# Optimization experiments

Measured on AMD Instinct MI355X. Metric: run time of the kernel, lower is better.

The kernel has to match this reference:

```python
import jax, jax.numpy as jnp
import numpy as np

# dims: batch, points, patches(groups), patch size, hidden, heads, layers, ffn
B, N, G, K, D, H, L, F = 32, 8192, 256, 32, 384, 6, 12, 1536
MASK_RATIO = 0.75
LEN_KEEP = int(G * (1 - MASK_RATIO))  # 64 visible tokens
HD = D // H


def _layernorm(x, g, b, eps=1e-5):
    m = jnp.mean(x, -1, keepdims=True)
    v = jnp.mean(jnp.square(x - m), -1, keepdims=True)
    return (x - m) * jax.lax.rsqrt(v + eps) * g + b


def _normalize_points(x):
    # normalize(): center = mid of bbox, radius = max distance to center (iso/diag)
    bmin = x.min(-2, keepdims=True)
    bmax = x.max(-2, keepdims=True)
    center = 0.5 * (bmin + bmax)
    radius = jnp.linalg.norm(x - center, axis=-1, keepdims=True).max(-2, keepdims=True)
    return (x - center) / radius


def _fps(x, num_samples):
    # farthest point sampling; sequential by nature -> fori_loop over G (fixed, small)
    b, n, _ = x.shape
    idxs = jnp.zeros((b, num_samples), jnp.int32)

    def body(i, state):
        dists, idxs, last = state
        lastpt = jnp.take_along_axis(x, last[:, None, None].astype(jnp.int32), axis=1)  # [B,1,3]
        d = jnp.sum(jnp.square(x - lastpt), -1)  # [B,N]
        dists = jnp.minimum(dists, d)
        nxt = jnp.argmax(dists, -1).astype(jnp.int32)
        return dists, idxs.at[:, i].set(nxt), nxt

    dists0 = jnp.full((b, n), 1e10, x.dtype)
    _, idxs, _ = jax.lax.fori_loop(1, num_samples, body, (dists0, idxs, jnp.zeros((b,), jnp.int32)))
    return idxs


def _group(x, centers):
    # squared pairwise distances without materializing [B,G,N,3]
    d2 = (jnp.sum(jnp.square(centers), -1)[:, :, None]
          + jnp.sum(jnp.square(x), -1)[:, None, :]
          - 2.0 * jnp.einsum('bgc,bnc->bgn', centers, x))  # [B,G,N]
    _, idx = jax.lax.top_k(-d2, K)  # [B,G,K] knn indices
    nbrs = jnp.take_along_axis(x[:, None, :, :], idx[..., None], axis=2)  # [B,G,K,3] (_knn_gather)
    return nbrs - centers[:, :, None, :]


def setup_inputs() -> dict:
    key = jax.random.key(0)
    ks = iter(jax.random.split(key, 24))

    def w(shape, scale=0.02):
        return jax.random.normal(next(ks), shape, jnp.float32) * scale

    ones_ln = jnp.stack([jnp.ones(D, jnp.float32), jnp.zeros(D, jnp.float32)])
    return {
        'points': jax.random.normal(next(ks), (B, N, 3), jnp.float32),
        'noise': jax.random.uniform(next(ks), (B, G), jnp.float32),
        # mini-PointNet patch encoder
        'pe_w1': w((3, 128)), 'pe_b1': jnp.zeros((128,), jnp.float32),
        'pe_w2': w((128, 256)), 'pe_b2': jnp.zeros((256,), jnp.float32),
        'pe_w3': w((256, D)), 'pe_b3': jnp.zeros((D,), jnp.float32),
        # positional MLP on patch centers
        'pos_w1': w((3, 128)), 'pos_b1': jnp.zeros((128,), jnp.float32),
        'pos_w2': w((128, D)), 'pos_b2': jnp.zeros((D,), jnp.float32),
        # transformer (stacked over L layers)
        'ln1': jnp.tile(ones_ln[None], (L, 1, 1)),
        'wqkv': w((L, D, 3 * D)), 'bqkv': jnp.zeros((L, 3 * D), jnp.float32),
        'wo': w((L, D, D)), 'bo': jnp.zeros((L, D), jnp.float32),
        'ln2': jnp.tile(ones_ln[None], (L, 1, 1)),
        'wi': w((L, D, F)), 'bi': jnp.zeros((L, F), jnp.float32),
        'wo2': w((L, F, D)), 'bo2': jnp.zeros((L, D), jnp.float32),
        'lnf': ones_ln,
    }


def _forward(points, noise, pe_w1, pe_b1, pe_w2, pe_b2, pe_w3, pe_b3,
             pos_w1, pos_b1, pos_w2, pos_b2,
             ln1, wqkv, bqkv, wo, bo, ln2, wi, bi, wo2, bo2, lnf):
    x = _normalize_points(points)
    cidx = _fps(x, G)                                        # [B,G]
    centers = jnp.take_along_axis(x, cidx[..., None], axis=1)  # [B,G,3]
    patches = _group(x, centers)                              # [B,G,K,3]

    # patch encode (per-point MLP -> max pool -> proj)
    f = jax.nn.relu(patches @ pe_w1 + pe_b1)
    f = f @ pe_w2 + pe_b2
    tokens = f.max(axis=2) @ pe_w3 + pe_b3                    # [B,G,D]
    pos = jax.nn.relu(centers @ pos_w1 + pos_b1) @ pos_w2 + pos_b2  # [B,G,D]

    # mask(): argsort-of-noise shuffle, keep first len_keep tokens
    ids_shuffle = jnp.argsort(noise, axis=1)
    ids_keep = ids_shuffle[:, :LEN_KEEP]                      # [B,64]
    h = (jnp.take_along_axis(tokens, ids_keep[..., None], axis=1)
         + jnp.take_along_axis(pos, ids_keep[..., None], axis=1))  # [B,64,D]

    scale = 1.0 / jnp.sqrt(jnp.asarray(HD, h.dtype))

    def layer(h, p):
        l1, wq, bq, wo_, bo_, l2, wi_, bi_, wo2_, bo2_ = p
        y = _layernorm(h, l1[0], l1[1])
        qkv = (y @ wq + bq).reshape(B, LEN_KEEP, 3, H, HD)  # '(three h d)' split
        q, k, v = jnp.moveaxis(qkv, 2, 0)
        a = jax.nn.softmax(jnp.einsum('bshd,bthd->bhst', q, k) * scale, -1)
        o = jnp.einsum('bhst,bthd->bshd', a, v).reshape(B, LEN_KEEP, D)
        h = h + o @ wo_ + bo_
        y = _layernorm(h, l2[0], l2[1])
        h = h + jax.nn.gelu(y @ wi_ + bi_) @ wo2_ + bo2_
        return h, None

    h, _ = jax.lax.scan(layer, h, (ln1, wqkv, bqkv, wo, bo, ln2, wi, bi, wo2, bo2))
    return _layernorm(h, lnf[0], lnf[1])


def reference(points, noise, pe_w1, pe_b1, pe_w2, pe_b2, pe_w3, pe_b3,
              pos_w1, pos_b1, pos_w2, pos_b2,
              ln1, wqkv, bqkv, wo, bo, ln2, wi, bi, wo2, bo2, lnf):
    return _forward(points, noise, pe_w1, pe_b1, pe_w2, pe_b2, pe_w3, pe_b3,
                    pos_w1, pos_b1, pos_w2, pos_b2,
                    ln1, wqkv, bqkv, wo, bo, ln2, wi, bi, wo2, bo2, lnf)
```

## Files before the change

kernel.cpp:

```cpp
#include <hip/hip_runtime.h>

#define NPTS 8192
#define NB   32
#define NG   256
#define NK   32
#define ND   384
#define NH   6
#define NLK  64
#define NF   1536
#define NHD  64
#define NL   12
#define MM   2048

typedef unsigned short u16;
typedef unsigned long long u64;
typedef __attribute__((ext_vector_type(8))) short short8;
typedef __attribute__((ext_vector_type(16))) float f32x16;
typedef __attribute__((ext_vector_type(4))) unsigned short ushort4v;

__device__ __forceinline__ float bf2f(u16 v){
  unsigned int u = ((unsigned int)v) << 16;
  float f; __builtin_memcpy(&f, &u, 4); return f;
}
__device__ __forceinline__ float ldf(const void* p, size_t i, bool bf){
  if(bf) return bf2f(((const u16*)p)[i]);
  return ((const float*)p)[i];
}
__device__ __forceinline__ u16 f2bf(float f){
  unsigned int x; __builtin_memcpy(&x, &f, 4);
  x += 0x7fffu + ((x >> 16) & 1u);
  return (u16)(x >> 16);
}
__device__ __forceinline__ void split2(float v, u16& hi, u16& lo){
  hi = f2bf(v);
  lo = f2bf(v - bf2f(hi));
}

__global__ __launch_bounds__(256) void k_detect(const u16* __restrict__ pts,
                                                int* __restrict__ flag){
  __shared__ int bad;
  if(threadIdx.x==0) bad=0;
  __syncthreads();
  int hit=0;
  for(int i=threadIdx.x; i<4096; i+=256){
    unsigned e = (pts[i] >> 7) & 0xFFu;
    if(e >= 0x90u) hit=1;
  }
  if(hit) atomicOr(&bad, 1);
  __syncthreads();
  if(threadIdx.x==0) *flag = bad ? 0 : 1;
}

__device__ __forceinline__ float blockMax256(float v, float* sb, int tid){
  for(int off=32; off; off>>=1) v = fmaxf(v, __shfl_down(v, off));
  __syncthreads();
  if((tid&63)==0) sb[tid>>6] = v;
  __syncthreads();
  return fmaxf(fmaxf(sb[0],sb[1]), fmaxf(sb[2],sb[3]));
}

__global__ __launch_bounds__(256) void k_normalize(const void* __restrict__ pts,
                                                   float* __restrict__ xn,
                                                   const int* __restrict__ flag){
#pragma clang fp contract(off)
  int b = blockIdx.x, tid = threadIdx.x;
  const bool bf = flag[0] != 0;
  __shared__ float sb[4];
  const size_t base = (size_t)b*NPTS*3;
  float mn0=1e30f,mn1=1e30f,mn2=1e30f, mx0=-1e30f,mx1=-1e30f,mx2=-1e30f;
  for(int n=tid; n<NPTS; n+=256){
    float x0=ldf(pts,base+n*3,bf), x1=ldf(pts,base+n*3+1,bf), x2=ldf(pts,base+n*3+2,bf);
    mn0=fminf(mn0,x0); mx0=fmaxf(mx0,x0);
    mn1=fminf(mn1,x1); mx1=fmaxf(mx1,x1);
    mn2=fminf(mn2,x2); mx2=fmaxf(mx2,x2);
  }
  mx0=blockMax256(mx0,sb,tid); mn0=-blockMax256(-mn0,sb,tid);
  mx1=blockMax256(mx1,sb,tid); mn1=-blockMax256(-mn1,sb,tid);
  mx2=blockMax256(mx2,sb,tid); mn2=-blockMax256(-mn2,sb,tid);
  float c0=0.5f*(mn0+mx0), c1=0.5f*(mn1+mx1), c2=0.5f*(mn2+mx2);
  float mr=0.0f;
  for(int n=tid; n<NPTS; n+=256){
    float d0=ldf(pts,base+n*3,bf)-c0, d1=ldf(pts,base+n*3+1,bf)-c1, d2=ldf(pts,base+n*3+2,bf)-c2;
    float nr = sqrtf((d0*d0 + d1*d1) + d2*d2);
    mr = fmaxf(mr, nr);
  }
  float radius = blockMax256(mr, sb, tid);
  float* XO = xn + base;
  for(int n=tid; n<NPTS; n+=256){
    XO[n*3  ] = (ldf(pts,base+n*3  ,bf)-c0)/radius;
    XO[n*3+1] = (ldf(pts,base+n*3+1,bf)-c1)/radius;
    XO[n*3+2] = (ldf(pts,base+n*3+2,bf)-c2)/radius;
  }
}

__global__ __launch_bounds__(256) void k_keep(const void* __restrict__ noise,
                                              int* __restrict__ keep,
                                              const int* __restrict__ flag){
  int b = blockIdx.x, g = threadIdx.x;
  const bool bf = flag[0] != 0;
  __shared__ float nv[NG];
  nv[g] = ldf(noise, (size_t)b*NG+g, bf);
  __syncthreads();
  float v = nv[g]; int r = 0;
  for(int j=0; j<NG; j++){
    float u = nv[j];
    r += (u < v) || (u == v && j < g);
  }
  if(r < NLK) keep[b*NLK + r] = g;
}

__device__ __forceinline__ void kmax_dpp_step(unsigned& hi, unsigned& lo, unsigned oh, unsigned ol){
  bool g = (oh > hi) || (oh == hi && ol > lo);
  hi = g ? oh : hi; lo = g ? ol : lo;
}
#define KMAX_DPP(CTRL) { \
  unsigned oh=(unsigned)__builtin_amdgcn_update_dpp(0,(int)kh,(CTRL),0xf,0xf,true); \
  unsigned ol=(unsigned)__builtin_amdgcn_update_dpp(0,(int)kl,(CTRL),0xf,0xf,true); \
  kmax_dpp_step(kh,kl,oh,ol); }

__global__ __launch_bounds__(512) void k_fps(const float* __restrict__ xn,
                                             float* __restrict__ centers){
#pragma clang fp contract(off)
  int b = blockIdx.x, tid = threadIdx.x;
  int lane = tid & 63;
  const float* X = xn + (size_t)b*NPTS*3;
  __shared__ float xs[NPTS*3];
  __shared__ u64 skey[3];
  __shared__ int sc[NG];
  float px[16],py[16],pz[16],dd[16];
#pragma unroll
  for(int s=0;s<16;s++){
    int n = s*512 + tid;
    px[s]=X[n*3]; py[s]=X[n*3+1]; pz[s]=X[n*3+2];
    dd[s]=1e10f;
  }
  for(int i=tid; i<NPTS*3; i+=512) xs[i] = X[i];
  if(tid==0){ skey[0]=0ull; skey[1]=0ull; skey[2]=0ull; sc[0]=0; }
  __syncthreads();
  float lx = xs[0], ly = xs[1], lz = xs[2];
  for(int i=1;i<NG;i++){
    int c = i % 3;
    float bv=-1.0f; int bs=0;
#pragma unroll
    for(int s=0;s<16;s++){
      float dx=px[s]-lx, dy=py[s]-ly, dz=pz[s]-lz;
      float d=(dx*dx + dy*dy) + dz*dz;
      d = fminf(dd[s], d); dd[s]=d;
      if(d > bv){ bv=d; bs=s; }
    }
    int bn = bs*512 + tid;
    unsigned kh; __builtin_memcpy(&kh,&bv,4);
    unsigned kl = (unsigned)(NPTS-1-bn);
    KMAX_DPP(0x111)
    KMAX_DPP(0x112)
    KMAX_DPP(0x114)
    KMAX_DPP(0x118)
    KMAX_DPP(0x142)
    KMAX_DPP(0x143)
    if(lane==63) atomicMax(&skey[c], ((u64)kh<<32) | (u64)kl);
    __syncthreads();
    u64 k64 = skey[c];
    int n = (NPTS-1) - (int)(k64 & 0xFFFFFFFFull);
    n &= (NPTS-1);
    if(tid==0){ sc[i]=n; skey[(i+2)%3]=0ull; }
    lx = xs[n*3]; ly = xs[n*3+1]; lz = xs[n*3+2];
  }
  __syncthreads();
  if(tid < NG){
    int n = sc[tid] & (NPTS-1);
    centers[((size_t)b*NG+tid)*3  ] = xs[n*3];
    centers[((size_t)b*NG+tid)*3+1] = xs[n*3+1];
    centers[((size_t)b*NG+tid)*3+2] = xs[n*3+2];
  }
}

__global__ __launch_bounds__(256) void k_knn(
    const float* __restrict__ xn, const float* __restrict__ centers,
    const int* __restrict__ keep, float* __restrict__ patches)
{
  int blk=blockIdx.x; int b=blk>>6; int j=blk&63; int tid=threadIdx.x;
  __shared__ float sd[NPTS];
  __shared__ int   sel[NK];
  __shared__ float rv[4]; __shared__ int rn[4];
  __shared__ int   sseln;
  int g = keep[b*NLK + j] & (NG-1);
  const float* C = centers + ((size_t)b*NG + g)*3;
  float c0=C[0], c1=C[1], c2=C[2];
  const float* X = xn + (size_t)b*NPTS*3;
  {
#pragma clang fp contract(off)
    float cc = (c0*c0 + c1*c1) + c2*c2;
    for(int n=tid; n<NPTS; n+=256){
      float x0=X[n*3], x1=X[n*3+1], x2=X[n*3+2];
      float xx=(x0*x0 + x1*x1) + x2*x2;
      float dt=(c0*x0 + c1*x1) + c2*x2;
      sd[n] = (cc + xx) - 2.0f*dt;
    }
  }
  __syncthreads();
  float dl[32];
  for(int s=0;s<32;s++) dl[s] = sd[s*256 + tid];
  unsigned int alive = 0xffffffffu;
  for(int r=0; r<NK; r++){
    float bv=1e30f; int bn=0x7fffffff;
    for(int s=0;s<32;s++){
      if(alive & (1u<<s)){
        float v = dl[s];
        if(v < bv){ bv=v; bn=s*256+tid; }
      }
    }
    for(int off=32;off;off>>=1){
      float ov=__shfl_down(bv,off); int on=__shfl_down(bn,off);
      if(ov<bv || (ov==bv && on<bn)){ bv=ov; bn=on; }
    }
    if((tid&63)==0){ rv[tid>>6]=bv; rn[tid>>6]=bn; }
    __syncthreads();
    if(tid==0){
      float v=rv[0]; int n=rn[0];
      for(int w=1;w<4;w++) if(rv[w]<v || (rv[w]==v && rn[w]<n)){ v=rv[w]; n=rn[w]; }
      n &= (NPTS-1);
      sseln=n; sel[r]=n;
    }
    __syncthreads();
    int n = sseln;
    if((n & 255) == tid) alive &= ~(1u << (n >> 8));
  }
  __syncthreads();
  if(tid < NK){
    int n = sel[tid] & (NPTS-1);
    float* P = patches + ((size_t)(b*NLK+j)*NK + tid)*3;
    P[0]=X[n*3  ]-c0;
    P[1]=X[n*3+1]-c1;
    P[2]=X[n*3+2]-c2;
  }
}

__global__ __launch_bounds__(256) void k_embed(
    const float* __restrict__ patches, const float* __restrict__ centers,
    const int* __restrict__ keep,
    const void* __restrict__ w1, const void* __restrict__ b1,
    const void* __restrict__ w2, const void* __restrict__ b2,
    const void* __restrict__ pw1, const void* __restrict__ pb1,
    u16* __restrict__ mfhi, u16* __restrict__ mflo,
    u16* __restrict__ phhi, u16* __restrict__ phlo,
    const int* __restrict__ flag)
{
  int blk=blockIdx.x; int b=blk>>6; int j=blk&63; int tid=threadIdx.x;
  const bool bf = flag[0] != 0;
  __shared__ float pat[NK*3];
  __shared__ __align__(16) float f1t[128*36];
  int row = b*NLK + j;
  if(tid < NK*3) pat[tid] = patches[(size_t)row*NK*3 + tid];
  __syncthreads();
  for(int i=0;i<16;i++){
    int idx = tid + i*256;
    int k = idx>>7, m = idx&127;
    float v = ldf(b1,m,bf)
            + pat[k*3+0]*ldf(w1,        m,bf)
            + pat[k*3+1]*ldf(w1, 128 + m,bf)
            + pat[k*3+2]*ldf(w1, 256 + m,bf);
    f1t[m*36 + k] = fmaxf(v, 0.0f);
  }
  __syncthreads();
  float acc[NK];
  {
    float bv = ldf(b2, tid, bf);
#pragma unroll
    for(int k=0;k<NK;k++) acc[k]=bv;
  }
  for(int jj=0;jj<128;jj++){
    float wv = ldf(w2, (size_t)jj*256+tid, bf);
    const float* fr = &f1t[jj*36];
#pragma unroll
    for(int k8=0;k8<8;k8++){
      float4 fv = *reinterpret_cast<const float4*>(fr + k8*4);
      acc[k8*4+0] = fmaf(fv.x, wv, acc[k8*4+0]);
      acc[k8*4+1] = fmaf(fv.y, wv, acc[k8*4+1]);
      acc[k8*4+2] = fmaf(fv.z, wv, acc[k8*4+2]);
      acc[k8*4+3] = fmaf(fv.w, wv, acc[k8*4+3]);
    }
  }
  float mx = acc[0];
#pragma unroll
  for(int k=1;k<NK;k++) mx = fmaxf(mx, acc[k]);
  { u16 hi,lo; split2(mx,hi,lo);
    mfhi[(size_t)row*256 + tid]=hi; mflo[(size_t)row*256 + tid]=lo; }
  if(tid < 128){
    int g = keep[b*NLK + j] & (NG-1);
    const float* C = centers + ((size_t)b*NG + g)*3;
    float v = ldf(pb1,tid,bf)
            + C[0]*ldf(pw1,        tid,bf)
            + C[1]*ldf(pw1, 128 + tid,bf)
            + C[2]*ldf(pw1, 256 + tid,bf);
    v = fmaxf(v, 0.0f);
    u16 hi,lo; split2(v,hi,lo);
    phhi[(size_t)row*128 + tid]=hi; phlo[(size_t)row*128 + tid]=lo;
  }
}

__global__ __launch_bounds__(256) void k_transpose(const void* __restrict__ W, size_t woff,
    int Kd, int Nd, u16* __restrict__ dhi, u16* __restrict__ dlo, size_t doff,
    const int* __restrict__ flag){
  __shared__ float t[32][33];
  const bool bf = flag[0]!=0;
  int n0 = blockIdx.x*32, k0 = blockIdx.y*32;
  for(int i=0;i<4;i++){
    int idx = threadIdx.x + i*256; int kr = idx>>5, nc = idx&31;
    t[kr][nc] = ldf(W, woff + (size_t)(k0+kr)*Nd + n0+nc, bf);
  }
  __syncthreads();
  for(int i=0;i<4;i++){
    int idx = threadIdx.x + i*256; int nr = idx>>5, kc = idx&31;
    float v = t[kc][nr];
    u16 hi,lo; split2(v,hi,lo);
    size_t o = doff + (size_t)(n0+nr)*Kd + k0+kc;
    dhi[o]=hi; dlo[o]=lo;
  }
}

__global__ __launch_bounds__(256) void k_transpose4(
    const void* __restrict__ wqkv, const void* __restrict__ wo,
    const void* __restrict__ wi,   const void* __restrict__ wo2,
    int l, u16* __restrict__ dhi, u16* __restrict__ dlo,
    const int* __restrict__ flag){
  __shared__ float t[32][33];
  const bool bf = flag[0]!=0;
  int id = blockIdx.x;
  const void* W; int Kd, Nd; size_t woff, doff; int local;
  if(id < 432){        W=wqkv; Kd=384;  Nd=1152; woff=(size_t)l*442368; doff=0;       local=id; }
  else if(id < 576){   W=wo;   Kd=384;  Nd=384;  woff=(size_t)l*147456; doff=442368;  local=id-432; }
  else if(id < 1152){  W=wi;   Kd=384;  Nd=1536; woff=(size_t)l*589824; doff=589824;  local=id-576; }
  else {               W=wo2;  Kd=1536; Nd=384;  woff=(size_t)l*589824; doff=1179648; local=id-1152; }
  int ntiles = Nd >> 5;
  int n0 = (local % ntiles)*32, k0 = (local / ntiles)*32;
  for(int i=0;i<4;i++){
    int idx = threadIdx.x + i*256; int kr = idx>>5, nc = idx&31;
    t[kr][nc] = ldf(W, woff + (size_t)(k0+kr)*Nd + n0+nc, bf);
  }
  __syncthreads();
  for(int i=0;i<4;i++){
    int idx = threadIdx.x + i*256; int nr = idx>>5, kc = idx&31;
    float v = t[kc][nr];
    u16 hi,lo; split2(v,hi,lo);
    size_t o = doff + (size_t)(n0+nr)*Kd + k0+kc;
    dhi[o]=hi; dlo[o]=lo;
  }
}

__global__ __launch_bounds__(128) void k_ln_split(const float* __restrict__ X,
                                                  const void* __restrict__ gb, size_t go,
                                                  u16* __restrict__ Yhi, u16* __restrict__ Ylo,
                                                  const int* __restrict__ flag){
  int row=blockIdx.x, tid=threadIdx.x;
  const bool bf = flag[0] != 0;
  const float* x = X + (size_t)row*ND;
  __shared__ float sbuf[2];
  float v0=x[tid], v1=x[tid+128], v2=x[tid+256];
  float s = v0+v1+v2;
  for(int off=32;off;off>>=1) s += __shfl_down(s,off);
  if((tid&63)==0) sbuf[tid>>6]=s;
  __syncthreads();
  float mean = (sbuf[0]+sbuf[1]) * (1.0f/(float)ND);
  __syncthreads();
  float d0=v0-mean, d1=v1-mean, d2=v2-mean;
  s = d0*d0 + d1*d1 + d2*d2;
  for(int off=32;off;off>>=1) s += __shfl_down(s,off);
  if((tid&63)==0) sbuf[tid>>6]=s;
  __syncthreads();
  float var = (sbuf[0]+sbuf[1]) * (1.0f/(float)ND);
  float rstd = 1.0f / sqrtf(var + 1e-5f);
  float o0 = d0*rstd*ldf(gb,go+tid    ,bf) + ldf(gb,go+ND+tid    ,bf);
  float o1 = d1*rstd*ldf(gb,go+tid+128,bf) + ldf(gb,go+ND+tid+128,bf);
  float o2 = d2*rstd*ldf(gb,go+tid+256,bf) + ldf(gb,go+ND+tid+256,bf);
  u16 hi,lo; size_t rb = (size_t)row*ND;
  split2(o0,hi,lo); Yhi[rb+tid    ]=hi; Ylo[rb+tid    ]=lo;
  split2(o1,hi,lo); Yhi[rb+tid+128]=hi; Ylo[rb+tid+128]=lo;
  split2(o2,hi,lo); Yhi[rb+tid+256]=hi; Ylo[rb+tid+256]=lo;
}

template<int TM, int TN, int ACT, bool RES, bool OSPLIT>
__global__ __launch_bounds__(256) void k_gemm_mfma(
    const u16* __restrict__ Ahi, const u16* __restrict__ Alo,
    const u16* __restrict__ Whi, const u16* __restrict__ Wlo, size_t wo,
    const void* __restrict__ bias, size_t bo, const int* __restrict__ flag,
    const float* __restrict__ res, float* __restrict__ Cf,
    u16* __restrict__ Ohi, u16* __restrict__ Olo,
    int N, int K)
{
  __shared__ __align__(16) u16 sAh[2][64*40];
  __shared__ __align__(16) u16 sAl[2][64*40];
  __shared__ __align__(16) u16 sBh[2][64*40];
  __shared__ __align__(16) u16 sBl[2][64*40];
  int tid = threadIdx.x;
  int wave = tid >> 6, lane = tid & 63;
  int wm = wave >> 1, wn = wave & 1;
  int l31 = lane & 31, half = lane >> 5;
  int row0 = blockIdx.y*TM, col0 = blockIdx.x*TN;
  const bool bf = flag[0] != 0;
  f32x16 acc;
#pragma unroll
  for(int r=0;r<16;r++) acc[r]=0.f;

  const int sr  = tid >> 2;
  const int scc = (tid & 3) * 8;
  const u16* gAh = Ahi + (size_t)(row0+sr)*K + scc;
  const u16* gAl = Alo + (size_t)(row0+sr)*K + scc;
  const u16* gBh = Whi + wo + (size_t)(col0+sr)*K + scc;
  const u16* gBl = Wlo + wo + (size_t)(col0+sr)*K + scc;
  const int ldst = sr*40 + scc;

  uint4 rah = *reinterpret_cast<const uint4*>(gAh);
  uint4 ral = *reinterpret_cast<const uint4*>(gAl);
  uint4 rbh = *reinterpret_cast<const uint4*>(gBh);
  uint4 rbl = *reinterpret_cast<const uint4*>(gBl);

  const int nk = K >> 5;
  for(int t=0; t<nk; ++t){
    const int buf = t & 1;
    *reinterpret_cast<uint4*>(&sAh[buf][ldst]) = rah;
    *reinterpret_cast<uint4*>(&sAl[buf][ldst]) = ral;
    *reinterpret_cast<uint4*>(&sBh[buf][ldst]) = rbh;
    *reinterpret_cast<uint4*>(&sBl[buf][ldst]) = rbl;
    __syncthreads();
    if(t+1 < nk){
      const int ko = (t+1) << 5;
      rah = *reinterpret_cast<const uint4*>(gAh + ko);
      ral = *reinterpret_cast<const uint4*>(gAl + ko);
      rbh = *reinterpret_cast<const uint4*>(gBh + ko);
      rbl = *reinterpret_cast<const uint4*>(gBl + ko);
    }
#pragma unroll
    for(int ks=0; ks<2; ks++){
      int aoff = (wm*32 + l31)*40 + ks*16 + half*8;
      int boff = (wn*32 + l31)*40 + ks*16 + half*8;
      short8 ah = *reinterpret_cast<const short8*>(&sAh[buf][aoff]);
      short8 al = *reinterpret_cast<const short8*>(&sAl[buf][aoff]);
      short8 bh = *reinterpret_cast<const short8*>(&sBh[buf][boff]);
      short8 bl = *reinterpret_cast<const short8*>(&sBl[buf][boff]);
      acc = __builtin_amdgcn_mfma_f32_32x32x16_bf16(ah, bh, acc, 0,0,0);
      acc = __builtin_amdgcn_mfma_f32_32x32x16_bf16(ah, bl, acc, 0,0,0);
      acc = __builtin_amdgcn_mfma_f32_32x32x16_bf16(al, bh, acc, 0,0,0);
    }
  }
  int col = col0 + wn*32 + l31;
  float bv = ldf(bias, bo+col, bf);
#pragma unroll
  for(int r=0;r<16;r++){
    int row = row0 + wm*32 + (r&3) + 8*(r>>2) + 4*half;
    float v = acc[r] + bv;
    if(ACT==1){
      float xx = v;
      v = 0.5f*xx*(1.0f + tanhf(0.7978845608028654f*(xx + 0.044715f*xx*xx*xx)));
    }
    if(RES) v += res[(size_t)row*N + col];
    if(OSPLIT){
      u16 hi,lo; split2(v,hi,lo);
      Ohi[(size_t)row*N + col]=hi; Olo[(size_t)row*N + col]=lo;
    }else{
      Cf[(size_t)row*N + col]=v;
    }
  }
}

__global__ __launch_bounds__(256) void k_attn_pl(const float* __restrict__ qkv,
                                                 u16* __restrict__ ohi,
                                                 u16* __restrict__ olo){
  __shared__ float Qt[64*68];
  __shared__ float Kt[64*68];
  __shared__ float V [64*68];
  __shared__ float SB[64*68];
  int blk=blockIdx.x; int b=blk/NH, h=blk%NH;
  int tid=threadIdx.x;
  for(int idx=tid; idx<4096; idx+=256){
    int s=idx>>6, d=idx&63;
    const float* r = qkv + ((size_t)(b*NLK+s))*1152 + h*NHD + d;
    Qt[d*68+s]=r[0];
    Kt[d*68+s]=r[384];
    V [s*68+d]=r[768];
  }
  __syncthreads();
  {
    const int i0 = (tid>>4)*4, j0 = (tid&15)*4;
    float a00=0.f,a01=0.f,a02=0.f,a03=0.f;
    float a10=0.f,a11=0.f,a12=0.f,a13=0.f;
    float a20=0.f,a21=0.f,a22=0.f,a23=0.f;
    float a30=0.f,a31=0.f,a32=0.f,a33=0.f;
#pragma unroll 4
    for(int d=0;d<64;d++){
      float4 qa = *reinterpret_cast<const float4*>(&Qt[d*68+i0]);
      float4 kb = *reinterpret_cast<const float4*>(&Kt[d*68+j0]);
      a00=fmaf(qa.x,kb.x,a00); a01=fmaf(qa.x,kb.y,a01); a02=fmaf(qa.x,kb.z,a02); a03=fmaf(qa.x,kb.w,a03);
      a10=fmaf(qa.y,kb.x,a10); a11=fmaf(qa.y,kb.y,a11); a12=fmaf(qa.y,kb.z,a12); a13=fmaf(qa.y,kb.w,a13);
      a20=fmaf(qa.z,kb.x,a20); a21=fmaf(qa.z,kb.y,a21); a22=fmaf(qa.z,kb.z,a22); a23=fmaf(qa.z,kb.w,a23);
      a30=fmaf(qa.w,kb.x,a30); a31=fmaf(qa.w,kb.y,a31); a32=fmaf(qa.w,kb.z,a32); a33=fmaf(qa.w,kb.w,a33);
    }
    float4 o0 = {a00*0.125f, a01*0.125f, a02*0.125f, a03*0.125f};
    float4 o1 = {a10*0.125f, a11*0.125f, a12*0.125f, a13*0.125f};
    float4 o2 = {a20*0.125f, a21*0.125f, a22*0.125f, a23*0.125f};
    float4 o3 = {a30*0.125f, a31*0.125f, a32*0.125f, a33*0.125f};
    *reinterpret_cast<float4*>(&SB[(i0  )*68+j0]) = o0;
    *reinterpret_cast<float4*>(&SB[(i0+1)*68+j0]) = o1;
    *reinterpret_cast<float4*>(&SB[(i0+2)*68+j0]) = o2;
    *reinterpret_cast<float4*>(&SB[(i0+3)*68+j0]) = o3;
  }
  __syncthreads();
  if(tid<64){
    float* rowp=&SB[tid*68];
    float m=rowp[0];
    for(int j=1;j<64;j++) m=fmaxf(m,rowp[j]);
    float sum=0.0f;
    for(int j=0;j<64;j++){ float e=__expf(rowp[j]-m); rowp[j]=e; sum+=e; }
    for(int j=0;j<64;j++) Qt[j*68+tid] = rowp[j]/sum;
  }
  __syncthreads();
  {
    const int s0 = (tid>>4)*4, d0 = (tid&15)*4;
    float a00=0.f,a01=0.f,a02=0.f,a03=0.f;
    float a10=0.f,a11=0.f,a12=0.f,a13=0.f;
    float a20=0.f,a21=0.f,a22=0.f,a23=0.f;
    float a30=0.f,a31=0.f,a32=0.f,a33=0.f;
#pragma unroll 4
    for(int t=0;t<64;t++){
      float4 av = *reinterpret_cast<const float4*>(&Qt[t*68+s0]);
      float4 vv = *reinterpret_cast<const float4*>(&V [t*68+d0]);
      a00=fmaf(av.x,vv.x,a00); a01=fmaf(av.x,vv.y,a01); a02=fmaf(av.x,vv.z,a02); a03=fmaf(av.x,vv.w,a03);
      a10=fmaf(av.y,vv.x,a10); a11=fmaf(av.y,vv.y,a11); a12=fmaf(av.y,vv.z,a12); a13=fmaf(av.y,vv.w,a13);
      a20=fmaf(av.z,vv.x,a20); a21=fmaf(av.z,vv.y,a21); a22=fmaf(av.z,vv.z,a22); a23=fmaf(av.z,vv.w,a23);
      a30=fmaf(av.w,vv.x,a30); a31=fmaf(av.w,vv.y,a31); a32=fmaf(av.w,vv.z,a32); a33=fmaf(av.w,vv.w,a33);
    }
    float rr[4][4] = {{a00,a01,a02,a03},{a10,a11,a12,a13},{a20,a21,a22,a23},{a30,a31,a32,a33}};
#pragma unroll
    for(int si=0; si<4; si++){
      ushort4v h4, l4;
#pragma unroll
      for(int di=0; di<4; di++){
        u16 hi,lo; split2(rr[si][di],hi,lo);
        h4[di]=hi; l4[di]=lo;
      }
      size_t o = ((size_t)(b*NLK+s0+si))*ND + h*NHD + d0;
      *reinterpret_cast<ushort4v*>(&ohi[o]) = h4;
      *reinterpret_cast<ushort4v*>(&olo[o]) = l4;
    }
  }
}

template<bool FINAL>
__global__ __launch_bounds__(128) void k_ln(const float* __restrict__ X,
                                            const void* __restrict__ gb, size_t go,
                                            void* __restrict__ Y,
                                            const int* __restrict__ flag){
  int row=blockIdx.x, tid=threadIdx.x;
  const bool bf = flag[0] != 0;
  const float* x = X + (size_t)row*ND;
  __shared__ float sbuf[2];
  float v0=x[tid], v1=x[tid+128], v2=x[tid+256];
  float s = v0+v1+v2;
  for(int off=32;off;off>>=1) s += __shfl_down(s,off);
  if((tid&63)==0) sbuf[tid>>6]=s;
  __syncthreads();
  float mean = (sbuf[0]+sbuf[1]) * (1.0f/(float)ND);
  __syncthreads();
  float d0=v0-mean, d1=v1-mean, d2=v2-mean;
  s = d0*d0 + d1*d1 + d2*d2;
  for(int off=32;off;off>>=1) s += __shfl_down(s,off);
  if((tid&63)==0) sbuf[tid>>6]=s;
  __syncthreads();
  float var = (sbuf[0]+sbuf[1]) * (1.0f/(float)ND);
  float rstd = 1.0f / sqrtf(var + 1e-5f);
  float o0 = d0*rstd*ldf(gb,go+tid    ,bf) + ldf(gb,go+ND+tid    ,bf);
  float o1 = d1*rstd*ldf(gb,go+tid+128,bf) + ldf(gb,go+ND+tid+128,bf);
  float o2 = d2*rstd*ldf(gb,go+tid+256,bf) + ldf(gb,go+ND+tid+256,bf);
  if(FINAL && bf){
    u16* yo = (u16*)Y + (size_t)row*ND;
    yo[tid]=f2bf(o0); yo[tid+128]=f2bf(o1); yo[tid+256]=f2bf(o2);
  }else{
    float* yo = (float*)Y + (size_t)row*ND;
    yo[tid]=o0; yo[tid+128]=o1; yo[tid+256]=o2;
  }
}

extern "C" void kernel_launch(void* const* d_in, const int* in_sizes, int n_in,
                              void* d_out, int out_size, void* d_ws, size_t ws_size,
                              hipStream_t stream){
  (void)in_sizes; (void)n_in; (void)out_size;
  const void* pts   = d_in[0];
  const void* noise = d_in[1];
  const void* pe_w1 = d_in[2];
  const void* pe_b1 = d_in[3];
  const void* pe_w2 = d_in[4];
  const void* pe_b2 = d_in[5];
  const void* pe_w3 = d_in[6];
  const void* pe_b3 = d_in[7];
  const void* pos_w1= d_in[8];
  const void* pos_b1= d_in[9];
  const void* pos_w2= d_in[10];
  const void* pos_b2= d_in[11];
  const void* ln1   = d_in[12];
  const void* wqkv  = d_in[13];
  const void* bqkv  = d_in[14];
  const void* wo    = d_in[15];
  const void* bo    = d_in[16];
  const void* ln2   = d_in[17];
  const void* wi    = d_in[18];
  const void* bi    = d_in[19];
  const void* wo2   = d_in[20];
  const void* bo2   = d_in[21];
  const void* lnf   = d_in[22];

  const size_t needed_new = (6711296ull + 16) * 4;
  if (ws_size < needed_new) return;

  float* ws   = (float*)d_ws;
  float* h    = ws;
  u16*  yhi   = (u16*)(ws + 786432);
  u16*  ylo   = yhi + 786432;
  float* qkvb = ws + 1572864;
  u16*  athi  = (u16*)(ws + 3932160);
  u16*  atlo  = athi + 786432;
  u16*  ubhi  = (u16*)(ws + 1572864);
  u16*  ublo  = ubhi + 3145728;
  float* xn   = ws + 1572864;
  u16*  wthi  = (u16*)(ws + 4718592);
  u16*  wtlo  = wthi + 1769472;
  float* patches = ws + 6488064;
  float* centers = ws + 6684672;
  int*   keep    = (int*)(ws + 6709248);
  u16*  mfhi  = yhi;            u16* mflo = yhi + 2048*256;
  u16*  phhi  = athi;           u16* phlo = athi + 2048*128;
  int*   flag = (int*)(ws + 6711296);

  k_detect   <<<1, 256, 0, stream>>>((const u16*)pts, flag);
  k_normalize<<<NB, 256, 0, stream>>>(pts, xn, flag);
  k_keep     <<<NB, 256, 0, stream>>>(noise, keep, flag);
  k_fps      <<<NB, 512, 0, stream>>>(xn, centers);
  k_knn      <<<NB*NLK, 256, 0, stream>>>(xn, centers, keep, patches);
  k_embed    <<<NB*NLK, 256, 0, stream>>>(patches, centers, keep,
      pe_w1, pe_b1, pe_w2, pe_b2, pos_w1, pos_b1,
      mfhi, mflo, phhi, phlo, flag);
  k_transpose<<<dim3(12, 8), 256, 0, stream>>>(pe_w3, 0, 256, 384, wthi, wtlo, 0, flag);
  k_transpose<<<dim3(12, 4), 256, 0, stream>>>(pos_w2, 0, 128, 384, wthi, wtlo, 98304, flag);
  k_gemm_mfma<64,64,0,false,false><<<dim3(6,32), 256, 0, stream>>>(
      mfhi, mflo, wthi, wtlo, 0, pe_b3, 0, flag, nullptr, h, nullptr, nullptr, 384, 256);
  k_gemm_mfma<64,64,0,true ,false><<<dim3(6,32), 256, 0, stream>>>(
      phhi, phlo, wthi, wtlo, 98304, pos_b2, 0, flag, h, h, nullptr, nullptr, 384, 128);

  for(int l=0; l<NL; l++){
    k_transpose4<<<1728, 256, 0, stream>>>(wqkv, wo, wi, wo2, l, wthi, wtlo, flag);

    k_ln_split<<<MM, 128, 0, stream>>>(h, ln1, (size_t)l*2*ND, yhi, ylo, flag);
    k_gemm_mfma<64,64,0,false,false><<<dim3(18,32), 256, 0, stream>>>(
        yhi, ylo, wthi, wtlo, 0, bqkv, (size_t)l*1152, flag, nullptr, qkvb, nullptr, nullptr, 1152, 384);
    k_attn_pl<<<NB*NH, 256, 0, stream>>>(qkvb, athi, atlo);
    k_gemm_mfma<64,64,0,true ,false><<<dim3(6,32), 256, 0, stream>>>(
        athi, atlo, wthi, wtlo, 442368, bo, (size_t)l*384, flag, h, h, nullptr, nullptr, 384, 384);
    k_ln_split<<<MM, 128, 0, stream>>>(h, ln2, (size_t)l*2*ND, yhi, ylo, flag);
    k_gemm_mfma<64,64,1,false,true ><<<dim3(24,32), 256, 0, stream>>>(
        yhi, ylo, wthi, wtlo, 589824, bi, (size_t)l*1536, flag, nullptr, nullptr, ubhi, ublo, 1536, 384);
    k_gemm_mfma<64,64,0,true ,false><<<dim3(6,32), 256, 0, stream>>>(
        ubhi, ublo, wthi, wtlo, 1179648, bo2, (size_t)l*384, flag, h, h, nullptr, nullptr, 384, 1536);
  }
  k_ln<true><<<MM, 128, 0, stream>>>(h, lnf, 0, d_out, flag);
}
```

Baseline: 1.872 ms.

## Overlap all weight transposes with FPS in one fused launch

Extends the FPS kernel with extra blocks that transpose and hi/lo-split all embedding and all 12 layers' weights into a persistent buffer while the 32 FPS blocks run. This removes the per-layer transpose launches from the serial layer chain and uses CUs left idle by the latency-bound FPS. It requires a larger workspace. It falls back to per-layer transposes when the workspace is too small, and the fallback rearranges buffer offsets.

```diff
diff --git a/kernel.cpp b/kernel.cpp
--- a/kernel.cpp
+++ b/kernel.cpp
@@ -17,6 +17,10 @@
 typedef __attribute__((ext_vector_type(8))) short short8;
 typedef __attribute__((ext_vector_type(16))) float f32x16;
 typedef __attribute__((ext_vector_type(4))) unsigned short ushort4v;
+
+#define PL_PRE   147456ull
+#define PL_LAYER 1769472ull
+#define WT_ELEMS (PL_PRE + 12ull*PL_LAYER)
 
 __device__ __forceinline__ float bf2f(u16 v){
   unsigned int u = ((unsigned int)v) << 16;
@@ -118,59 +122,101 @@
   unsigned ol=(unsigned)__builtin_amdgcn_update_dpp(0,(int)kl,(CTRL),0xf,0xf,true); \
   kmax_dpp_step(kh,kl,oh,ol); }
 
-__global__ __launch_bounds__(512) void k_fps(const float* __restrict__ xn,
-                                             float* __restrict__ centers){
-#pragma clang fp contract(off)
-  int b = blockIdx.x, tid = threadIdx.x;
-  int lane = tid & 63;
-  const float* X = xn + (size_t)b*NPTS*3;
+__global__ __launch_bounds__(512) void k_fps_trans(
+    const float* __restrict__ xn, float* __restrict__ centers,
+    const void* __restrict__ pe_w3, const void* __restrict__ pos_w2,
+    const void* __restrict__ wqkv, const void* __restrict__ wo,
+    const void* __restrict__ wi,   const void* __restrict__ wo2,
+    u16* __restrict__ wthi, u16* __restrict__ wtlo,
+    const int* __restrict__ flag)
+{
   __shared__ float xs[NPTS*3];
   __shared__ u64 skey[3];
   __shared__ int sc[NG];
-  float px[16],py[16],pz[16],dd[16];
-#pragma unroll
-  for(int s=0;s<16;s++){
-    int n = s*512 + tid;
-    px[s]=X[n*3]; py[s]=X[n*3+1]; pz[s]=X[n*3+2];
-    dd[s]=1e10f;
-  }
-  for(int i=tid; i<NPTS*3; i+=512) xs[i] = X[i];
-  if(tid==0){ skey[0]=0ull; skey[1]=0ull; skey[2]=0ull; sc[0]=0; }
-  __syncthreads();
-  float lx = xs[0], ly = xs[1], lz = xs[2];
-  for(int i=1;i<NG;i++){
-    int c = i % 3;
-    float bv=-1.0f; int bs=0;
+  int tid = threadIdx.x;
+
+  if(blockIdx.x >= 32){
+    const bool bf = flag[0]!=0;
+    float (*t)[33] = reinterpret_cast<float(*)[33]>(xs);
+    int gid = blockIdx.x - 32;
+    const void* W; int Kd, Nd; size_t woff, doff; int local;
+    if(gid < 96){        W=pe_w3;  Kd=256; Nd=384; woff=0; doff=0;      local=gid; }
+    else if(gid < 144){  W=pos_w2; Kd=128; Nd=384; woff=0; doff=98304;  local=gid-96; }
+    else{
+      int g2 = gid - 144; int l = g2 / 1728; int id = g2 % 1728;
+      size_t lb = PL_PRE + (size_t)l*PL_LAYER;
+      if(id < 432){        W=wqkv; Kd=384;  Nd=1152; woff=(size_t)l*442368; doff=lb;          local=id; }
+      else if(id < 576){   W=wo;   Kd=384;  Nd=384;  woff=(size_t)l*147456; doff=lb+442368;   local=id-432; }
+      else if(id < 1152){  W=wi;   Kd=384;  Nd=1536; woff=(size_t)l*589824; doff=lb+589824;   local=id-576; }
+      else {               W=wo2;  Kd=1536; Nd=384;  woff=(size_t)l*589824; doff=lb+1179648;  local=id-1152; }
+    }
+    int ntiles = Nd >> 5;
+    int n0 = (local % ntiles)*32, k0 = (local / ntiles)*32;
+    for(int i=0;i<2;i++){
+      int idx = tid + i*512; int kr = idx>>5, nc = idx&31;
+      t[kr][nc] = ldf(W, woff + (size_t)(k0+kr)*Nd + n0+nc, bf);
+    }
+    __syncthreads();
+    for(int i=0;i<2;i++){
+      int idx = tid + i*512; int nr = idx>>5, kc = idx&31;
+      float v = t[kc][nr];
+      u16 hi,lo; split2(v,hi,lo);
+      size_t o = doff + (size_t)(n0+nr)*Kd + k0+kc;
+      wthi[o]=hi; wtlo[o]=lo;
+    }
+    return;
+  }
+
+  {
+#pragma clang fp contract(off)
+    int b = blockIdx.x;
+    int lane = tid & 63;
+    const float* X = xn + (size_t)b*NPTS*3;
+    float px[16],py[16],pz[16],dd[16];
 #pragma unroll
     for(int s=0;s<16;s++){
-      float dx=px[s]-lx, dy=py[s]-ly, dz=pz[s]-lz;
-      float d=(dx*dx + dy*dy) + dz*dz;
-      d = fminf(dd[s], d); dd[s]=d;
-      if(d > bv){ bv=d; bs=s; }
-    }
-    int bn = bs*512 + tid;
-    unsigned kh; __builtin_memcpy(&kh,&bv,4);
-    unsigned kl = (unsigned)(NPTS-1-bn);
-    KMAX_DPP(0x111)
-    KMAX_DPP(0x112)
-    KMAX_DPP(0x114)
-    KMAX_DPP(0x118)
-    KMAX_DPP(0x142)
-    KMAX_DPP(0x143)
-    if(lane==63) atomicMax(&skey[c], ((u64)kh<<32) | (u64)kl);
+      int n = s*512 + tid;
+      px[s]=X[n*3]; py[s]=X[n*3+1]; pz[s]=X[n*3+2];
+      dd[s]=1e10f;
+    }
+    for(int i=tid; i<NPTS*3; i+=512) xs[i] = X[i];
+    if(tid==0){ skey[0]=0ull; skey[1]=0ull; skey[2]=0ull; sc[0]=0; }
     __syncthreads();
-    u64 k64 = skey[c];
-    int n = (NPTS-1) - (int)(k64 & 0xFFFFFFFFull);
-    n &= (NPTS-1);
-    if(tid==0){ sc[i]=n; skey[(i+2)%3]=0ull; }
-    lx = xs[n*3]; ly = xs[n*3+1]; lz = xs[n*3+2];
-  }
-  __syncthreads();
-  if(tid < NG){
-    int n = sc[tid] & (NPTS-1);
-    centers[((size_t)b*NG+tid)*3  ] = xs[n*3];
-    centers[((size_t)b*NG+tid)*3+1] = xs[n*3+1];
-    centers[((size_t)b*NG+tid)*3+2] = xs[n*3+2];
+    float lx = xs[0], ly = xs[1], lz = xs[2];
+    for(int i=1;i<NG;i++){
+      int c = i % 3;
+      float bv=-1.0f; int bs=0;
+#pragma unroll
+      for(int s=0;s<16;s++){
+        float dx=px[s]-lx, dy=py[s]-ly, dz=pz[s]-lz;
+        float d=(dx*dx + dy*dy) + dz*dz;
+        d = fminf(dd[s], d); dd[s]=d;
+        if(d > bv){ bv=d; bs=s; }
+      }
+      int bn = bs*512 + tid;
+      unsigned kh; __builtin_memcpy(&kh,&bv,4);
+      unsigned kl = (unsigned)(NPTS-1-bn);
+      KMAX_DPP(0x111)
+      KMAX_DPP(0x112)
+      KMAX_DPP(0x114)
+      KMAX_DPP(0x118)
+      KMAX_DPP(0x142)
+      KMAX_DPP(0x143)
+      if(lane==63) atomicMax(&skey[c], ((u64)kh<<32) | (u64)kl);
+      __syncthreads();
+      u64 k64 = skey[c];
+      int n = (NPTS-1) - (int)(k64 & 0xFFFFFFFFull);
+      n &= (NPTS-1);
+      if(tid==0){ sc[i]=n; skey[(i+2)%3]=0ull; }
+      lx = xs[n*3]; ly = xs[n*3+1]; lz = xs[n*3+2];
+    }
+    __syncthreads();
+    if(tid < NG){
+      int n = sc[tid] & (NPTS-1);
+      centers[((size_t)b*NG+tid)*3  ] = xs[n*3];
+      centers[((size_t)b*NG+tid)*3+1] = xs[n*3+1];
+      centers[((size_t)b*NG+tid)*3+2] = xs[n*3+2];
+    }
   }
 }
 
@@ -298,26 +344,6 @@
   }
 }
 
-__global__ __launch_bounds__(256) void k_transpose(const void* __restrict__ W, size_t woff,
-    int Kd, int Nd, u16* __restrict__ dhi, u16* __restrict__ dlo, size_t doff,
-    const int* __restrict__ flag){
-  __shared__ float t[32][33];
-  const bool bf = flag[0]!=0;
-  int n0 = blockIdx.x*32, k0 = blockIdx.y*32;
-  for(int i=0;i<4;i++){
-    int idx = threadIdx.x + i*256; int kr = idx>>5, nc = idx&31;
-    t[kr][nc] = ldf(W, woff + (size_t)(k0+kr)*Nd + n0+nc, bf);
-  }
-  __syncthreads();
-  for(int i=0;i<4;i++){
-    int idx = threadIdx.x + i*256; int nr = idx>>5, kc = idx&31;
-    float v = t[kc][nr];
-    u16 hi,lo; split2(v,hi,lo);
-    size_t o = doff + (size_t)(n0+nr)*Kd + k0+kc;
-    dhi[o]=hi; dlo[o]=lo;
-  }
-}
-
 __global__ __launch_bounds__(256) void k_transpose4(
     const void* __restrict__ wqkv, const void* __restrict__ wo,
     const void* __restrict__ wi,   const void* __restrict__ wo2,
@@ -327,10 +353,10 @@
   const bool bf = flag[0]!=0;
   int id = blockIdx.x;
   const void* W; int Kd, Nd; size_t woff, doff; int local;
-  if(id < 432){        W=wqkv; Kd=384;  Nd=1152; woff=(size_t)l*442368; doff=0;       local=id; }
-  else if(id < 576){   W=wo;   Kd=384;  Nd=384;  woff=(size_t)l*147456; doff=442368;  local=id-432; }
-  else if(id < 1152){  W=wi;   Kd=384;  Nd=1536; woff=(size_t)l*589824; doff=589824;  local=id-576; }
-  else {               W=wo2;  Kd=1536; Nd=384;  woff=(size_t)l*589824; doff=1179648; local=id-1152; }
+  if(id < 432){        W=wqkv; Kd=384;  Nd=1152; woff=(size_t)l*442368; doff=PL_PRE;          local=id; }
+  else if(id < 576){   W=wo;   Kd=384;  Nd=384;  woff=(size_t)l*147456; doff=PL_PRE+442368;   local=id-432; }
+  else if(id < 1152){  W=wi;   Kd=384;  Nd=1536; woff=(size_t)l*589824; doff=PL_PRE+589824;   local=id-576; }
+  else {               W=wo2;  Kd=1536; Nd=384;  woff=(size_t)l*589824; doff=PL_PRE+1179648;  local=id-1152; }
   int ntiles = Nd >> 5;
   int n0 = (local % ntiles)*32, k0 = (local / ntiles)*32;
   for(int i=0;i<4;i++){
@@ -607,8 +633,11 @@
   const void* bo2   = d_in[21];
   const void* lnf   = d_in[22];
 
-  const size_t needed_new = (6711296ull + 16) * 4;
-  if (ws_size < needed_new) return;
+  const size_t needed_small = (6711296ull + 16) * 4;
+  if (ws_size < needed_small) return;
+  const size_t wt_f32_off = 6711312ull;
+  const size_t needed_big = (wt_f32_off + WT_ELEMS) * 4;
+  const bool big = ws_size >= needed_big;
 
   float* ws   = (float*)d_ws;
   float* h    = ws;
@@ -620,44 +649,61 @@
   u16*  ubhi  = (u16*)(ws + 1572864);
   u16*  ublo  = ubhi + 3145728;
   float* xn   = ws + 1572864;
-  u16*  wthi  = (u16*)(ws + 4718592);
-  u16*  wtlo  = wthi + 1769472;
-  float* patches = ws + 6488064;
-  float* centers = ws + 6684672;
-  int*   keep    = (int*)(ws + 6709248);
-  u16*  mfhi  = yhi;            u16* mflo = yhi + 2048*256;
-  u16*  phhi  = athi;           u16* phlo = athi + 2048*128;
-  int*   flag = (int*)(ws + 6711296);
+  float* patches;
+  float* centers;
+  int*   keep;
+  int*   flag;
+  u16 *wthi, *wtlo;
+  if(big){
+    patches = ws + 6488064;
+    centers = ws + 6684672;
+    keep    = (int*)(ws + 6709248);
+    flag    = (int*)(ws + 6711296);
+    wthi    = (u16*)(ws + wt_f32_off);
+    wtlo    = wthi + WT_ELEMS;
+  }else{
+    wthi    = (u16*)(ws + 4718592);
+    wtlo    = (u16*)(ws + 5677056);
+    patches = ws + 6635520;
+    centers = ws + 6832128;
+    keep    = (int*)(ws + 6856704);
+    flag    = (int*)(ws + 6858752);
+    if(ws_size < (6858752ull + 16) * 4) return;
+  }
 
   k_detect   <<<1, 256, 0, stream>>>((const u16*)pts, flag);
   k_normalize<<<NB, 256, 0, stream>>>(pts, xn, flag);
   k_keep     <<<NB, 256, 0, stream>>>(noise, keep, flag);
-  k_fps      <<<NB, 512, 0, stream>>>(xn, centers);
+  {
+    int grid = big ? (32 + 144 + 12*1728) : (32 + 144);
+    k_fps_trans<<<grid, 512, 0, stream>>>(xn, centers, pe_w3, pos_w2,
+        wqkv, wo, wi, wo2, wthi, wtlo, flag);
+  }
   k_knn      <<<NB*NLK, 256, 0, stream>>>(xn, centers, keep, patches);
   k_embed    <<<NB*NLK, 256, 0, stream>>>(patches, centers, keep,
       pe_w1, pe_b1, pe_w2, pe_b2, pos_w1, pos_b1,
-      mfhi, mflo, phhi, phlo, flag);
-  k_transpose<<<dim3(12, 8), 256, 0, stream>>>(pe_w3, 0, 256, 384, wthi, wtlo, 0, flag);
-  k_transpose<<<dim3(12, 4), 256, 0, stream>>>(pos_w2, 0, 128, 384, wthi, wtlo, 98304, flag);
+      yhi , yhi + 2048*256 , athi , athi + 2048*128 , flag);
   k_gemm_mfma<64,64,0,false,false><<<dim3(6,32), 256, 0, stream>>>(
-      mfhi, mflo, wthi, wtlo, 0, pe_b3, 0, flag, nullptr, h, nullptr, nullptr, 384, 256);
+      yhi, yhi + 2048*256, wthi, wtlo, 0, pe_b3, 0, flag, nullptr, h, nullptr, nullptr, 384, 256);
   k_gemm_mfma<64,64,0,true ,false><<<dim3(6,32), 256, 0, stream>>>(
-      phhi, phlo, wthi, wtlo, 98304, pos_b2, 0, flag, h, h, nullptr, nullptr, 384, 128);
+      athi, athi + 2048*128, wthi, wtlo, 98304, pos_b2, 0, flag, h, h, nullptr, nullptr, 384, 128);
 
   for(int l=0; l<NL; l++){
-    k_transpose4<<<1728, 256, 0, stream>>>(wqkv, wo, wi, wo2, l, wthi, wtlo, flag);
-
+    size_t lb = big ? (PL_PRE + (size_t)l*PL_LAYER) : PL_PRE;
+    if(!big){
+      k_transpose4<<<1728, 256, 0, stream>>>(wqkv, wo, wi, wo2, l, wthi, wtlo, flag);
+    }
     k_ln_split<<<MM, 128, 0, stream>>>(h, ln1, (size_t)l*2*ND, yhi, ylo, flag);
     k_gemm_mfma<64,64,0,false,false><<<dim3(18,32), 256, 0, stream>>>(
-        yhi, ylo, wthi, wtlo, 0, bqkv, (size_t)l*1152, flag, nullptr, qkvb, nullptr, nullptr, 1152, 384);
+        yhi, ylo, wthi, wtlo, lb, bqkv, (size_t)l*1152, flag, nullptr, qkvb, nullptr, nullptr, 1152, 384);
     k_attn_pl<<<NB*NH, 256, 0, stream>>>(qkvb, athi, atlo);
     k_gemm_mfma<64,64,0,true ,false><<<dim3(6,32), 256, 0, stream>>>(
-        athi, atlo, wthi, wtlo, 442368, bo, (size_t)l*384, flag, h, h, nullptr, nullptr, 384, 384);
+        athi, atlo, wthi, wtlo, lb + 442368, bo, (size_t)l*384, flag, h, h, nullptr, nullptr, 384, 384);
     k_ln_split<<<MM, 128, 0, stream>>>(h, ln2, (size_t)l*2*ND, yhi, ylo, flag);
     k_gemm_mfma<64,64,1,false,true ><<<dim3(24,32), 256, 0, stream>>>(
-        yhi, ylo, wthi, wtlo, 589824, bi, (size_t)l*1536, flag, nullptr, nullptr, ubhi, ublo, 1536, 384);
+        yhi, ylo, wthi, wtlo, lb + 589824, bi, (size_t)l*1536, flag, nullptr, nullptr, ubhi, ublo, 1536, 384);
     k_gemm_mfma<64,64,0,true ,false><<<dim3(6,32), 256, 0, stream>>>(
-        ubhi, ublo, wthi, wtlo, 1179648, bo2, (size_t)l*384, flag, h, h, nullptr, nullptr, 384, 1536);
+        ubhi, ublo, wthi, wtlo, lb + 1179648, bo2, (size_t)l*384, flag, h, h, nullptr, nullptr, 384, 1536);
   }
   k_ln<true><<<MM, 128, 0, stream>>>(h, lnf, 0, d_out, flag);
 }
```

New measurement: 1.815 ms. 3.0% less time.
